# Optimization experiments

Hardware: AMD Instinct MI355X
Metric: run time of the kernel (lower is better)

The kernel has to match this reference:

```python
import jax, jax.numpy as jnp
import numpy as np

N_NODES = 100000
N_EDGES = 3200000
IN_FEATS = 128
HIDDEN = 64
N_CLASSES = 16


def gcn_conv(x, src, dst, W, b, num_nodes):
    """PyG GCNConv (default settings): add self-loops, symmetric norm,
    linear transform, scatter-sum aggregation at dst, then bias."""
    # degree counts include self-loops (fill value 1.0)
    deg = jnp.zeros((num_nodes,), x.dtype).at[dst].add(1.0) + 1.0
    dinv = jax.lax.rsqrt(deg)  # deg >= 1, no inf handling needed
    h = x @ W  # [N, out]
    # edge messages: norm(src,dst) * h[src], aggregated at dst
    norm = dinv[src] * dinv[dst]  # [E]
    msg = h[src] * norm[:, None]  # [E, out]
    out = jax.ops.segment_sum(msg, dst, num_segments=num_nodes)
    # self-loop contribution: norm = dinv[i]^2
    out = out + h * (dinv * dinv)[:, None]
    return out + b


def setup_inputs() -> dict:
    key = jax.random.key(0)
    k1, k2, k3, k4 = jax.random.split(key, 4)
    x = jax.random.normal(k1, (N_NODES, IN_FEATS), dtype=jnp.float32)
    edge_index = jax.random.randint(k2, (2, N_EDGES), 0, N_NODES, dtype=jnp.int64)
    W1 = jax.random.normal(k3, (IN_FEATS, HIDDEN), dtype=jnp.float32) * (1.0 / np.sqrt(IN_FEATS))
    b1 = jnp.zeros((HIDDEN,), jnp.float32)
    W2 = jax.random.normal(k4, (HIDDEN, N_CLASSES), dtype=jnp.float32) * (1.0 / np.sqrt(HIDDEN))
    b2 = jnp.zeros((N_CLASSES,), jnp.float32)
    return {"x": x, "edge_index": edge_index, "W1": W1, "b1": b1, "W2": W2, "b2": b2}


def reference(x, edge_index, W1, b1, W2, b2):
    src, dst = edge_index[0], edge_index[1]
    h = gcn_conv(x, src, dst, W1, b1, N_NODES)
    h = jax.nn.relu(h)  # dropout is identity in eval mode
    out = gcn_conv(h, src, dst, W2, b2, N_NODES)
    return out
```

## Files before the change

### kernel.cpp

```cpp
#include <hip/hip_runtime.h>
#include <hip/hip_fp16.h>
#include <stdint.h>

#define N_NODES   100000
#define N_HALF    50000
#define N_EDGES   3200000
#define F_IN      128
#define F_HID     64
#define F_OUT     16

typedef _Float16 h2v __attribute__((ext_vector_type(2)));
typedef _Float16 h4v __attribute__((ext_vector_type(4)));
typedef float    f4v __attribute__((ext_vector_type(4)));

#define BSHIFT    8
#define NBUCK     391
#define NBLK_P    800
#define CHUNK_E   (N_EDGES / NBLK_P)
#define PSTRIDE   9856

#define G1_TM     64
#define G1_BLOCKS ((N_NODES + G1_TM - 1) / G1_TM)
#define XS_LD     68

#define OFF_RS       0
#define OFF_LEN      400000
#define OFF_DINV     800000
#define OFF_GCNT     1200000
#define OFF_CSR      1201616
#define OFF_HS1      8909008
#define OFF_OUT1A    21709008
#define OFF_OUT1B    34509008
#define OFF_HS2      47309008
#define OFF_PAIRS    OFF_OUT1A

__global__ __launch_bounds__(256, 4) void k_partition(const void* __restrict__ ei,
                                                      int* __restrict__ gcnt,
                                                      unsigned* __restrict__ pairs) {
    __shared__ unsigned long long st[CHUNK_E];
    __shared__ int h[NBUCK];
    __shared__ int cur[NBUCK];
    __shared__ int is64s;
    int t = threadIdx.x;
    if (t < 64) {
        const unsigned* u = (const unsigned*)ei;
        unsigned lo = u[2 * t], hi = u[2 * t + 1];
        int bad = (hi != 0u || lo >= 100000u) ? 1 : 0;
        unsigned long long mask = __ballot(bad);
        if (t == 0) is64s = (mask == 0ull);
    }
    for (int i = t; i < NBUCK; i += 256) h[i] = 0;
    __syncthreads();
    int shift = 2 + is64s;
    const char* sp = (const char*)ei;
    const char* dp = sp + ((size_t)N_EDGES << shift);
#define LDS_IDX(p, e) __builtin_nontemporal_load((const unsigned*)((p) + ((size_t)(e) << shift)))
    int base = blockIdx.x * CHUNK_E;
    int i = t;
    for (; i + 768 < CHUNK_E; i += 1024) {
        int e0 = base + i, e1 = e0 + 256, e2 = e0 + 512, e3 = e0 + 768;
        unsigned s0 = LDS_IDX(sp, e0), s1 = LDS_IDX(sp, e1);
        unsigned s2 = LDS_IDX(sp, e2), s3 = LDS_IDX(sp, e3);
        unsigned d0 = LDS_IDX(dp, e0), d1 = LDS_IDX(dp, e1);
        unsigned d2 = LDS_IDX(dp, e2), d3 = LDS_IDX(dp, e3);
        st[i]       = ((unsigned long long)s0 << 32) | d0;
        st[i + 256] = ((unsigned long long)s1 << 32) | d1;
        st[i + 512] = ((unsigned long long)s2 << 32) | d2;
        st[i + 768] = ((unsigned long long)s3 << 32) | d3;
        atomicAdd(&h[d0 >> BSHIFT], 1);
        atomicAdd(&h[d1 >> BSHIFT], 1);
        atomicAdd(&h[d2 >> BSHIFT], 1);
        atomicAdd(&h[d3 >> BSHIFT], 1);
    }
    for (; i < CHUNK_E; i += 256) {
        unsigned s = LDS_IDX(sp, base + i);
        unsigned d = LDS_IDX(dp, base + i);
        st[i] = ((unsigned long long)s << 32) | d;
        atomicAdd(&h[d >> BSHIFT], 1);
    }
#undef LDS_IDX
    __syncthreads();
    for (int j = t; j < NBUCK; j += 256) {
        int c = h[j];
        cur[j] = c ? atomicAdd(&gcnt[j], c) : 0;
    }
    __syncthreads();
    i = t;
    for (; i + 768 < CHUNK_E; i += 1024) {
        unsigned long long v0 = st[i],       v1 = st[i + 256];
        unsigned long long v2 = st[i + 512], v3 = st[i + 768];
        unsigned d0 = (unsigned)v0, d1 = (unsigned)v1;
        unsigned d2 = (unsigned)v2, d3 = (unsigned)v3;
        int p0 = atomicAdd(&cur[d0 >> BSHIFT], 1);
        int p1 = atomicAdd(&cur[d1 >> BSHIFT], 1);
        int p2 = atomicAdd(&cur[d2 >> BSHIFT], 1);
        int p3 = atomicAdd(&cur[d3 >> BSHIFT], 1);
        if (p0 < PSTRIDE) pairs[(d0 >> BSHIFT) * PSTRIDE + p0] = ((unsigned)(v0 >> 32) << 8) | (d0 & 255u);
        if (p1 < PSTRIDE) pairs[(d1 >> BSHIFT) * PSTRIDE + p1] = ((unsigned)(v1 >> 32) << 8) | (d1 & 255u);
        if (p2 < PSTRIDE) pairs[(d2 >> BSHIFT) * PSTRIDE + p2] = ((unsigned)(v2 >> 32) << 8) | (d2 & 255u);
        if (p3 < PSTRIDE) pairs[(d3 >> BSHIFT) * PSTRIDE + p3] = ((unsigned)(v3 >> 32) << 8) | (d3 & 255u);
    }
    for (; i < CHUNK_E; i += 256) {
        unsigned long long v = st[i];
        unsigned d = (unsigned)v;
        int b = d >> BSHIFT;
        int p = atomicAdd(&cur[b], 1);
        if (p < PSTRIDE)
            pairs[b * PSTRIDE + p] = ((unsigned)(v >> 32) << 8) | (d & 255u);
    }
}

__global__ __launch_bounds__(512) void k_build(const unsigned* __restrict__ pairs,
                                               const int* __restrict__ gcnt,
                                               int* __restrict__ rowstart,
                                               int* __restrict__ lens,
                                               float* __restrict__ dinv,
                                               unsigned short* __restrict__ csr) {
    __shared__ unsigned prS[PSTRIDE];
    __shared__ unsigned short csrS[PSTRIDE];
    __shared__ int c0S[256], c1S[256], scanS[256], pos0[256], pos1[256];
    __shared__ int totpadS;
    int b = blockIdx.x, t = threadIdx.x;
    if (t < 256) { c0S[t] = 0; c1S[t] = 0; }
    __syncthreads();
    int tot = gcnt[b]; if (tot > PSTRIDE) tot = PSTRIDE;
    int base = b * PSTRIDE;
    for (int i = t; i < tot; i += 512) {
        unsigned pr = __builtin_nontemporal_load(pairs + base + i);
        prS[i] = pr;
        if ((pr >> 8) < (unsigned)N_HALF) atomicAdd(&c0S[pr & 255u], 1);
        else                              atomicAdd(&c1S[pr & 255u], 1);
    }
    __syncthreads();
    int tpad = 0, p0a = 0;
    if (t < 256) {
        p0a = (c0S[t] + 3) & ~3;
        tpad = p0a + ((c1S[t] + 3) & ~3);
        scanS[t] = tpad;
    }
    __syncthreads();
    for (int off = 1; off < 256; off <<= 1) {
        int add = 0;
        if (t < 256 && t >= off) add = scanS[t - off];
        __syncthreads();
        if (t < 256) scanS[t] += add;
        __syncthreads();
    }
    if (t < 256) {
        int rs = scanS[t] - tpad;
        pos0[t] = rs;
        pos1[t] = rs + p0a;
        int d = (b << BSHIFT) + t;
        if (d < N_NODES) {
            rowstart[d] = base + rs;
            lens[d] = c0S[t] | (c1S[t] << 16);
            dinv[d] = rsqrtf((float)(c0S[t] + c1S[t]) + 1.0f);
        }
        if (t == 255) totpadS = scanS[255];
    }
    __syncthreads();
    for (int i = t; i < tot; i += 512) {
        unsigned pr = prS[i];
        unsigned s = pr >> 8;
        int d = pr & 255u;
        if (s < (unsigned)N_HALF) {
            int p = atomicAdd(&pos0[d], 1);
            csrS[p] = (unsigned short)s;
        } else {
            int p = atomicAdd(&pos1[d], 1);
            csrS[p] = (unsigned short)(s - N_HALF);
        }
    }
    __syncthreads();
    int nchunk = (totpadS + 7) >> 3;
    uint4* dst = (uint4*)(csr + base);
    const uint4* srcp = (const uint4*)csrS;
    for (int i = t; i < nchunk; i += 512) dst[i] = srcp[i];
}

__global__ __launch_bounds__(256, 4) void k_gemm1(const float* __restrict__ x,
                                                  const float* __restrict__ W1,
                                                  const float* __restrict__ dinv,
                                                  __half* __restrict__ hs1) {
    __shared__ float xsT[32 * XS_LD];
    __shared__ float ws[32 * 64];
    int t = threadIdx.x;
    int nblock = blockIdx.x * G1_TM;
    int ng = t >> 4, og = t & 15;
    int n0 = ng * 4;
    float acc[4][4] = {};

    int nl = t >> 2;
    int koff = (t & 3) * 8;
    int snode = nblock + nl;

    for (int chunk = 0; chunk < 4; ++chunk) {
        int kbase = chunk * 32;
        {
            f4v v0, v1;
            if (snode < N_NODES) {
                const f4v* src = (const f4v*)(x + (size_t)snode * F_IN + kbase + koff);
                v0 = __builtin_nontemporal_load(src);
                v1 = __builtin_nontemporal_load(src + 1);
            } else {
                v0 = (f4v){0.f, 0.f, 0.f, 0.f};
                v1 = v0;
            }
#pragma unroll
            for (int i = 0; i < 4; ++i) {
                xsT[(koff + i) * XS_LD + nl]     = v0[i];
                xsT[(koff + 4 + i) * XS_LD + nl] = v1[i];
            }
        }
        {
            const float4* wsrc = (const float4*)(W1 + kbase * F_HID);
            float4* wdst = (float4*)ws;
            wdst[t]       = wsrc[t];
            wdst[256 + t] = wsrc[256 + t];
        }
        __syncthreads();

#pragma unroll 8
        for (int k = 0; k < 32; ++k) {
            float4 a = *(const float4*)(xsT + k * XS_LD + n0);
            float4 bv = *(const float4*)(ws + k * 64 + og * 4);
            float aa[4] = {a.x, a.y, a.z, a.w};
            float bb[4] = {bv.x, bv.y, bv.z, bv.w};
#pragma unroll
            for (int i = 0; i < 4; ++i)
#pragma unroll
                for (int j = 0; j < 4; ++j)
                    acc[i][j] += aa[i] * bb[j];
        }
        __syncthreads();
    }

#pragma unroll
    for (int i = 0; i < 4; ++i) {
        int node = nblock + n0 + i;
        if (node < N_NODES) {
            float dv = dinv[node];
            union { __half2 h[2]; float2 f; } u;
            u.h[0] = __floats2half2_rn(acc[i][0] * dv, acc[i][1] * dv);
            u.h[1] = __floats2half2_rn(acc[i][2] * dv, acc[i][3] * dv);
            *(float2*)(hs1 + ((size_t)(og >> 3) * N_NODES + node) * 32 + (og & 7) * 4) = u.f;
        }
    }
}

__global__ __launch_bounds__(256) void k_agg1(const __half* __restrict__ hs1,
                                              const unsigned short* __restrict__ csr,
                                              const int* __restrict__ rowstart,
                                              const int* __restrict__ lens,
                                              __half* __restrict__ out1a,
                                              __half* __restrict__ out1b) {
    int bid = blockIdx.x;
    int combo = bid & 3;
    int chunk = combo & 1, half = combo >> 1;
    int nb = bid >> 2;
    int w = threadIdx.x >> 6, lane = threadIdx.x & 63;
    int slot = lane >> 3, fp = lane & 7;
    int n = nb * 32 + w * 8 + slot;
    const char* T = (const char*)hs1
                  + (size_t)chunk * ((size_t)N_NODES * 64)
                  + (size_t)half * ((size_t)N_HALF * 64);
    unsigned fo = fp * 8u;
    int rs = rowstart[n];
    int L = lens[n];
    int c0 = L & 0xffff;
    int start = half ? (rs + ((c0 + 3) & ~3)) : rs;
    int c = half ? (L >> 16) : c0;
    h4v a0 = {(_Float16)0.f, (_Float16)0.f, (_Float16)0.f, (_Float16)0.f};
    h4v a1 = a0, a2 = a0, a3 = a0;
    const unsigned long long* Q = (const unsigned long long*)csr;
    int q0 = start >> 2;
    int nq = c >> 2;
#define ROW1(idx) (*(const h4v*)(T + (unsigned)(idx) * 64u + fo))
    int q = 0;
    unsigned long long ea = 0ull, eb = 0ull;
    if (q + 2 <= nq) { ea = Q[q0]; eb = Q[q0 + 1]; }
    while (q + 2 <= nq) {
        unsigned long long ca = ea, cb = eb;
        q += 2;
        if (q + 2 <= nq) { ea = Q[q0 + q]; eb = Q[q0 + q + 1]; }
        h4v t0 = ROW1(ca & 0xffffu);
        h4v t1 = ROW1((ca >> 16) & 0xffffu);
        h4v t2 = ROW1((ca >> 32) & 0xffffu);
        h4v t3 = ROW1(ca >> 48);
        h4v t4 = ROW1(cb & 0xffffu);
        h4v t5 = ROW1((cb >> 16) & 0xffffu);
        h4v t6 = ROW1((cb >> 32) & 0xffffu);
        h4v t7 = ROW1(cb >> 48);
        a0 += t0; a1 += t1; a2 += t2; a3 += t3;
        a0 += t4; a1 += t5; a2 += t6; a3 += t7;
    }
    if (q < nq) {
        unsigned long long e = Q[q0 + q];
        a0 += ROW1(e & 0xffffu);
        a1 += ROW1((e >> 16) & 0xffffu);
        a2 += ROW1((e >> 32) & 0xffffu);
        a3 += ROW1(e >> 48);
    }
    for (int j = start + (nq << 2); j < start + c; ++j)
        a0 += ROW1(csr[j]);
    if ((n >= N_HALF) == (half != 0))
        a1 += ROW1(n - half * N_HALF);
#undef ROW1
    float s0 = ((float)a0[0] + (float)a1[0]) + ((float)a2[0] + (float)a3[0]);
    float s1 = ((float)a0[1] + (float)a1[1]) + ((float)a2[1] + (float)a3[1]);
    float s2 = ((float)a0[2] + (float)a1[2]) + ((float)a2[2] + (float)a3[2]);
    float s3 = ((float)a0[3] + (float)a1[3]) + ((float)a2[3] + (float)a3[3]);
    union { __half2 h[2]; float2 f; } u;
    u.h[0] = __floats2half2_rn(s0, s1);
    u.h[1] = __floats2half2_rn(s2, s3);
    __half* dst = (half ? out1b : out1a) + (size_t)n * F_HID + chunk * 32 + fp * 4;
    *(float2*)dst = u.f;
}

__global__ __launch_bounds__(256) void k_gemm2(const __half* __restrict__ out1a,
                                               const __half* __restrict__ out1b,
                                               const float* __restrict__ W2,
                                               const float* __restrict__ dinv,
                                               const float* __restrict__ b1,
                                               __half* __restrict__ hs2) {
    __shared__ float ws[F_HID * F_OUT];
    __shared__ float b1s[F_HID];
    int t = threadIdx.x;
    ((float4*)ws)[t] = ((const float4*)W2)[t];
    if (t < 16) ((float4*)b1s)[t] = ((const float4*)b1)[t];
    __syncthreads();
    int tid = blockIdx.x * 256 + t;
    int n = tid >> 2;
    if (n >= N_NODES) return;
    int cq = (tid & 3) << 2;
    float dv = dinv[n];
    const h2v* A = (const h2v*)(out1a + (size_t)n * F_HID);
    const h2v* B = (const h2v*)(out1b + (size_t)n * F_HID);
    float4 acc = make_float4(0.f, 0.f, 0.f, 0.f);
#pragma unroll 4
    for (int k4 = 0; k4 < 16; ++k4) {
        h2v pa0 = A[k4 * 2], pa1 = A[k4 * 2 + 1];
        h2v pb0 = B[k4 * 2], pb1 = B[k4 * 2 + 1];
        float h0 = fmaxf(dv * ((float)pa0.x + (float)pb0.x) + b1s[k4 * 4 + 0], 0.f);
        float h1 = fmaxf(dv * ((float)pa0.y + (float)pb0.y) + b1s[k4 * 4 + 1], 0.f);
        float h2 = fmaxf(dv * ((float)pa1.x + (float)pb1.x) + b1s[k4 * 4 + 2], 0.f);
        float h3 = fmaxf(dv * ((float)pa1.y + (float)pb1.y) + b1s[k4 * 4 + 3], 0.f);
        float4 w0 = *(const float4*)(ws + (k4 * 4 + 0) * F_OUT + cq);
        float4 w1 = *(const float4*)(ws + (k4 * 4 + 1) * F_OUT + cq);
        float4 w2 = *(const float4*)(ws + (k4 * 4 + 2) * F_OUT + cq);
        float4 w3 = *(const float4*)(ws + (k4 * 4 + 3) * F_OUT + cq);
        acc.x += h0 * w0.x + h1 * w1.x + h2 * w2.x + h3 * w3.x;
        acc.y += h0 * w0.y + h1 * w1.y + h2 * w2.y + h3 * w3.y;
        acc.z += h0 * w0.z + h1 * w1.z + h2 * w2.z + h3 * w3.z;
        acc.w += h0 * w0.w + h1 * w1.w + h2 * w2.w + h3 * w3.w;
    }
    union { __half2 h2x[2]; float2 f; } u;
    u.h2x[0] = __floats2half2_rn(acc.x * dv, acc.y * dv);
    u.h2x[1] = __floats2half2_rn(acc.z * dv, acc.w * dv);
    *(float2*)(hs2 + (size_t)n * F_OUT + cq) = u.f;
}

__global__ __launch_bounds__(128) void k_agg2(const __half* __restrict__ hs2,
                                              const unsigned short* __restrict__ csr,
                                              const int* __restrict__ rowstart,
                                              const int* __restrict__ lens,
                                              const float* __restrict__ dinv,
                                              const float* __restrict__ b2,
                                              float* __restrict__ out) {
    int w = threadIdx.x >> 6, lane = threadIdx.x & 63;
    int slot = lane >> 2, fp = lane & 3;
    int n = blockIdx.x * 32 + w * 16 + slot;
    unsigned fo = fp * 8u;
    int rs = rowstart[n];
    int L = lens[n];
    int c0 = L & 0xffff, c1 = L >> 16;
    const unsigned long long* Q = (const unsigned long long*)csr;
    h4v a0 = {(_Float16)0.f, (_Float16)0.f, (_Float16)0.f, (_Float16)0.f};
    h4v a1 = a0, a2 = a0, a3 = a0;
#pragma unroll
    for (int half = 0; half < 2; ++half) {
        const char* T = (const char*)hs2 + (size_t)half * ((size_t)N_HALF * 32);
        int start = half ? (rs + ((c0 + 3) & ~3)) : rs;
        int c = half ? c1 : c0;
        int q0 = start >> 2;
        int nq = c >> 2;
#define ROW2(idx) (*(const h4v*)(T + (unsigned)(idx) * 32u + fo))
        int q = 0;
        unsigned long long ea = 0ull, eb = 0ull;
        if (q + 2 <= nq) { ea = Q[q0]; eb = Q[q0 + 1]; }
        while (q + 2 <= nq) {
            unsigned long long ca = ea, cb = eb;
            q += 2;
            if (q + 2 <= nq) { ea = Q[q0 + q]; eb = Q[q0 + q + 1]; }
            h4v t0 = ROW2(ca & 0xffffu);
            h4v t1 = ROW2((ca >> 16) & 0xffffu);
            h4v t2 = ROW2((ca >> 32) & 0xffffu);
            h4v t3 = ROW2(ca >> 48);
            h4v t4 = ROW2(cb & 0xffffu);
            h4v t5 = ROW2((cb >> 16) & 0xffffu);
            h4v t6 = ROW2((cb >> 32) & 0xffffu);
            h4v t7 = ROW2(cb >> 48);
            a0 += t0; a1 += t1; a2 += t2; a3 += t3;
            a0 += t4; a1 += t5; a2 += t6; a3 += t7;
        }
        if (q < nq) {
            unsigned long long e = Q[q0 + q];
            a0 += ROW2(e & 0xffffu);
            a1 += ROW2((e >> 16) & 0xffffu);
            a2 += ROW2((e >> 32) & 0xffffu);
            a3 += ROW2(e >> 48);
        }
        for (int j = start + (nq << 2); j < start + c; ++j)
            a0 += ROW2(csr[j]);
#undef ROW2
    }
    a1 += *(const h4v*)((const char*)hs2 + (unsigned)n * 32u + fo);
    float dv = dinv[n];
    int fb = fp * 4;
    float s0 = ((float)a0[0] + (float)a1[0]) + ((float)a2[0] + (float)a3[0]);
    float s1 = ((float)a0[1] + (float)a1[1]) + ((float)a2[1] + (float)a3[1]);
    float s2 = ((float)a0[2] + (float)a1[2]) + ((float)a2[2] + (float)a3[2]);
    float s3 = ((float)a0[3] + (float)a1[3]) + ((float)a2[3] + (float)a3[3]);
    float ox0 = dv * s0 + b2[fb + 0];
    float ox1 = dv * s1 + b2[fb + 1];
    float ox2 = dv * s2 + b2[fb + 2];
    float ox3 = dv * s3 + b2[fb + 3];
    float4* dst = (float4*)(out + (size_t)n * F_OUT + fb);
    *dst = make_float4(ox0, ox1, ox2, ox3);
}

extern "C" void kernel_launch(void* const* d_in, const int* in_sizes, int n_in,
                              void* d_out, int out_size, void* d_ws, size_t ws_size,
                              hipStream_t stream) {
    const float* x  = (const float*)d_in[0];
    const void*  ei = d_in[1];
    const float* W1 = (const float*)d_in[2];
    const float* b1 = (const float*)d_in[3];
    const float* W2 = (const float*)d_in[4];
    const float* b2 = (const float*)d_in[5];
    float* out = (float*)d_out;

    char* ws = (char*)d_ws;
    int*            rowstart = (int*)(ws + OFF_RS);
    int*            lens     = (int*)(ws + OFF_LEN);
    float*          dinv     = (float*)(ws + OFF_DINV);
    int*            gcnt     = (int*)(ws + OFF_GCNT);
    unsigned short* csr      = (unsigned short*)(ws + OFF_CSR);
    __half*         hs1      = (__half*)(ws + OFF_HS1);
    __half*         out1a    = (__half*)(ws + OFF_OUT1A);
    __half*         out1b    = (__half*)(ws + OFF_OUT1B);
    __half*         hs2      = (__half*)(ws + OFF_HS2);
    unsigned*       pairs    = (unsigned*)(ws + OFF_PAIRS);

    (void)hipMemsetAsync(gcnt, 0, NBUCK * sizeof(int), stream);
    k_partition<<<NBLK_P, 256, 0, stream>>>(ei, gcnt, pairs);
    k_build    <<<NBUCK, 512, 0, stream>>>(pairs, gcnt, rowstart, lens, dinv, csr);

    k_gemm1<<<G1_BLOCKS, 256, 0, stream>>>(x, W1, dinv, hs1);
    k_agg1 <<<12500, 256, 0, stream>>>(hs1, csr, rowstart, lens, out1a, out1b);
    k_gemm2<<<(N_NODES * 4 + 255) / 256, 256, 0, stream>>>(out1a, out1b, W2, dinv, b1, hs2);
    k_agg2 <<<3125, 128, 0, stream>>>(hs2, csr, rowstart, lens, dinv, b2, out);
}
```

Before: 282.9 us.

## Rewrite first-layer GEMM with fp16 MFMA 16x16x32 instructions

The first-layer dense transform x@W1 moves from a scalar FP32 register-tiled GEMM to MFMA matrix-core instructions. W1 is staged once per block into LDS as fp16 in an MFMA-friendly layout, and x rows are converted to fp16 in registers. The goal is to cut ALU time and LDS traffic so the kernel is bounded by loading x. In exchange, inputs are rounded to fp16 before multiplication, and the output stores become scalar 2-byte writes that are less coalesced.

Result: faster. 270.1 us (-4.5%).

```diff
diff --git a/kernel.cpp b/kernel.cpp
--- a/kernel.cpp
+++ b/kernel.cpp
@@ -11,6 +11,7 @@
 
 typedef _Float16 h2v __attribute__((ext_vector_type(2)));
 typedef _Float16 h4v __attribute__((ext_vector_type(4)));
+typedef _Float16 h8v __attribute__((ext_vector_type(8)));
 typedef float    f4v __attribute__((ext_vector_type(4)));
 
 #define BSHIFT    8
@@ -21,7 +22,6 @@
 
 #define G1_TM     64
 #define G1_BLOCKS ((N_NODES + G1_TM - 1) / G1_TM)
-#define XS_LD     68
 
 #define OFF_RS       0
 #define OFF_LEN      400000
@@ -182,68 +182,51 @@
                                                   const float* __restrict__ W1,
                                                   const float* __restrict__ dinv,
                                                   __half* __restrict__ hs1) {
-    __shared__ float xsT[32 * XS_LD];
-    __shared__ float ws[32 * 64];
+    __shared__ _Float16 W1s[F_IN * F_HID];
     int t = threadIdx.x;
+    for (int idx = t; idx < F_IN * F_HID; idx += 256) {
+        int k = idx >> 6, n = idx & 63;
+        float v = W1[idx];
+        int kc = k >> 5, ko = (k >> 3) & 3, j = k & 7;
+        int nt = n >> 4, c = n & 15;
+        W1s[((kc * 4 + ko) * 4 + nt) * 128 + c * 8 + j] = (_Float16)v;
+    }
+    __syncthreads();
+    int w = t >> 6, l = t & 63;
+    int lm = l & 15, lk = l >> 4;
     int nblock = blockIdx.x * G1_TM;
-    int ng = t >> 4, og = t & 15;
-    int n0 = ng * 4;
-    float acc[4][4] = {};
-
-    int nl = t >> 2;
-    int koff = (t & 3) * 8;
-    int snode = nblock + nl;
-
-    for (int chunk = 0; chunk < 4; ++chunk) {
-        int kbase = chunk * 32;
-        {
-            f4v v0, v1;
-            if (snode < N_NODES) {
-                const f4v* src = (const f4v*)(x + (size_t)snode * F_IN + kbase + koff);
-                v0 = __builtin_nontemporal_load(src);
-                v1 = __builtin_nontemporal_load(src + 1);
-            } else {
-                v0 = (f4v){0.f, 0.f, 0.f, 0.f};
-                v1 = v0;
-            }
-#pragma unroll
-            for (int i = 0; i < 4; ++i) {
-                xsT[(koff + i) * XS_LD + nl]     = v0[i];
-                xsT[(koff + 4 + i) * XS_LD + nl] = v1[i];
-            }
-        }
-        {
-            const float4* wsrc = (const float4*)(W1 + kbase * F_HID);
-            float4* wdst = (float4*)ws;
-            wdst[t]       = wsrc[t];
-            wdst[256 + t] = wsrc[256 + t];
-        }
-        __syncthreads();
-
-#pragma unroll 8
-        for (int k = 0; k < 32; ++k) {
-            float4 a = *(const float4*)(xsT + k * XS_LD + n0);
-            float4 bv = *(const float4*)(ws + k * 64 + og * 4);
-            float aa[4] = {a.x, a.y, a.z, a.w};
-            float bb[4] = {bv.x, bv.y, bv.z, bv.w};
-#pragma unroll
-            for (int i = 0; i < 4; ++i)
-#pragma unroll
-                for (int j = 0; j < 4; ++j)
-                    acc[i][j] += aa[i] * bb[j];
-        }
-        __syncthreads();
-    }
-
-#pragma unroll
-    for (int i = 0; i < 4; ++i) {
-        int node = nblock + n0 + i;
+    int anode = nblock + w * 16 + lm;
+    int anodec = anode < N_NODES ? anode : N_NODES - 1;
+    f4v acc[4] = {};
+    const h8v* Bp = (const h8v*)W1s;
+#pragma unroll
+    for (int kc = 0; kc < 4; ++kc) {
+        const f4v* src = (const f4v*)(x + (size_t)anodec * F_IN + kc * 32 + lk * 8);
+        f4v v0 = __builtin_nontemporal_load(src);
+        f4v v1 = __builtin_nontemporal_load(src + 1);
+        h8v a;
+#pragma unroll
+        for (int i = 0; i < 4; ++i) {
+            a[i]     = (_Float16)v0[i];
+            a[i + 4] = (_Float16)v1[i];
+        }
+#pragma unroll
+        for (int nt = 0; nt < 4; ++nt) {
+            h8v b = Bp[((kc * 4 + lk) * 4 + nt) * 16 + lm];
+            acc[nt] = __builtin_amdgcn_mfma_f32_16x16x32_f16(a, b, acc[nt], 0, 0, 0);
+        }
+    }
+#pragma unroll
+    for (int r = 0; r < 4; ++r) {
+        int node = nblock + w * 16 + lk * 4 + r;
         if (node < N_NODES) {
             float dv = dinv[node];
-            union { __half2 h[2]; float2 f; } u;
-            u.h[0] = __floats2half2_rn(acc[i][0] * dv, acc[i][1] * dv);
-            u.h[1] = __floats2half2_rn(acc[i][2] * dv, acc[i][3] * dv);
-            *(float2*)(hs1 + ((size_t)(og >> 3) * N_NODES + node) * 32 + (og & 7) * 4) = u.f;
+#pragma unroll
+            for (int nt = 0; nt < 4; ++nt) {
+                float val = acc[nt][r] * dv;
+                hs1[((size_t)(nt >> 1) * N_NODES + node) * 32 + (nt & 1) * 16 + lm] =
+                    __float2half(val);
+            }
         }
     }
 }
```
